# Kernel tuning notes

Hardware: AMD Instinct MI355X
Metric: run time of the kernel (lower is better)

Reference implementation:

```python
import jax, jax.numpy as jnp
import numpy as np

B, U, F = 32768, 256, 256  # batch, units, input features
LR = 0.01                  # inner_lr
EPS = 1e-3                 # TF LayerNormalization default epsilon


def _layer_norm(x, gamma, beta):
    m = jnp.mean(x, axis=-1, keepdims=True)
    v = jnp.var(x, axis=-1, keepdims=True)
    return (x - m) * jax.lax.rsqrt(v + EPS) * gamma + beta


def _enc(W1, b1, W2, b2, u):
    # mlp_2 inner encoder: Dense(4U, gelu-exact) -> Dense(U)
    return jax.nn.gelu(u @ W1 + b1, approximate=False) @ W2 + b2


def setup_inputs() -> dict:
    key = jax.random.key(0)
    ks = jax.random.split(key, 12)
    def w(k, shape):
        fan_in = shape[0]
        return jax.random.normal(k, shape, jnp.float32) / np.sqrt(fan_in)
    return {
        "x": jax.random.normal(ks[0], (B, F), jnp.float32),
        "h_prev": jax.random.normal(ks[1], (B, U), jnp.float32),
        "W_phi": w(ks[2], (F + U, U)), "b_phi": jnp.zeros((U,), jnp.float32),
        "W_psi": w(ks[3], (F + U, U)), "b_psi": jnp.zeros((U,), jnp.float32),
        "W1": w(ks[4], (U, 4 * U)), "b1": jnp.zeros((4 * U,), jnp.float32),
        "W2": w(ks[5], (4 * U, U)), "b2": jnp.zeros((U,), jnp.float32),
        "W_g": w(ks[6], (U, U)), "g_bias": jnp.zeros((U,), jnp.float32),
        "ln_gamma": jnp.ones((U,), jnp.float32), "ln_beta": jnp.zeros((U,), jnp.float32),
        "W_h": w(ks[7], (U, U)), "h_bias": jnp.zeros((U,), jnp.float32),
    }


def reference(x, h_prev, W_phi, b_phi, W_psi, b_psi, W1, b1, W2, b2,
              W_g, g_bias, ln_gamma, ln_beta, W_h, h_bias):
    z = jnp.concatenate([x, h_prev], axis=-1)          # [B, F+U]
    phi = z @ W_phi + b_phi                            # [B, U], also the inner target

    def inner_loss(params):
        W1_, b1_, W2_, b2_ = params
        r = _enc(W1_, b1_, W2_, b2_, phi) @ W_g + g_bias
        r = _layer_norm(r, ln_gamma, ln_beta)
        return jnp.mean(jnp.square(r - phi)), r

    params = (W1, b1, W2, b2)
    # inner_iterations = 1: one SGD step on the inner-encoder weights only
    (_, recon), grads = jax.value_and_grad(inner_loss, has_aux=True)(params)
    params = tuple(p - LR * g for p, g in zip(params, grads))

    psi = z @ W_psi + b_psi                            # [B, U]
    feat = _enc(*params, psi) + 0.1 * recon            # updated encoder on psi
    out = feat @ W_h + h_bias                          # new hidden / cell output
    return out
```

## Files before the change

### kernel.cpp

```cpp
#include <hip/hip_runtime.h>
#include <math.h>

#define B_N 32768
#define U_N 256
#define H_N 1024
#define LR_C 0.01f
#define EPS_C 1e-3f

typedef unsigned short ushort_t;
typedef unsigned int uint_t;
using frag8 = __attribute__((ext_vector_type(8))) short;
using f32x4 = __attribute__((ext_vector_type(4))) float;

__device__ __forceinline__ float erf_fast(float y) {
    float ay = fabsf(y);
    float t = __builtin_amdgcn_rcpf(fmaf(0.3275911f, ay, 1.0f));
    float p = fmaf(1.061405429f, t, -1.453152027f);
    p = fmaf(p, t, 1.421413741f);
    p = fmaf(p, t, -0.284496736f);
    p = fmaf(p, t, 0.254829592f);
    p = p * t;
    float e = __expf(-ay * ay);
    float r = fmaf(-p, e, 1.0f);
    return copysignf(r, y);
}
__device__ __forceinline__ float gelu_f(float x) {
    return 0.5f * x * (1.0f + erf_fast(x * 0.7071067811865475f));
}
__device__ __forceinline__ void gelu_pair(float x, float& g, float& d) {
    float ay = fabsf(x) * 0.7071067811865475f;
    float t = __builtin_amdgcn_rcpf(fmaf(0.3275911f, ay, 1.0f));
    float p = fmaf(1.061405429f, t, -1.453152027f);
    p = fmaf(p, t, 1.421413741f);
    p = fmaf(p, t, -0.284496736f);
    p = fmaf(p, t, 0.254829592f);
    p = p * t;
    float e = __expf(-ay * ay);
    float er = copysignf(fmaf(-p, e, 1.0f), x);
    float c = 0.5f * (1.0f + er);
    g = x * c;
    d = fmaf(x * 0.3989422804014327f, e, c);
}
__device__ __forceinline__ void splitf(float v, ushort_t& h, ushort_t& l) {
    uint_t u = __float_as_uint(v);
    h = (ushort_t)(u >> 16);
    float r = v - __uint_as_float(u & 0xFFFF0000u);
    uint_t ru = __float_as_uint(r);
    l = (ushort_t)((ru + 0x7FFFu + ((ru >> 16) & 1u)) >> 16);
}
__device__ __forceinline__ ushort_t cvt_rne(float v) {
    uint_t u = __float_as_uint(v);
    return (ushort_t)((u + 0x7FFFu + ((u >> 16) & 1u)) >> 16);
}
__device__ __forceinline__ float bf2f(ushort_t u) {
    return __uint_as_float((uint_t)u << 16);
}
__device__ __forceinline__ void unpack2(uint_t pa, uint_t pb, uint_t& hw, uint_t& lw) {
    hw = __builtin_amdgcn_perm(pb, pa, 0x07060302u);
    lw = __builtin_amdgcn_perm(pb, pa, 0x05040100u);
}
__device__ __forceinline__ size_t swz(int n, int k, int K) {
    return (size_t)n * K +
           (size_t)((k & ~31) | ((((k >> 3) & 3) ^ ((n >> 1) & 3)) << 3) | (k & 7));
}
__device__ __forceinline__ void gload16(const ushort_t* g, ushort_t* l) {
    __builtin_amdgcn_global_load_lds(
        (const __attribute__((address_space(1))) void*)g,
        (__attribute__((address_space(3))) void*)l, 16, 0, 0);
}

#define EPI_NONE 0
#define EPI_GELU 1
#define EPI_ADDS 3

#define BEP_P   0
#define BEP_PT  1
#define BEP_A1  2
#define BEP_DAT 3

template<int ACONCAT, int APACK, int EPI, int OPACK>
__global__ __launch_bounds__(256)
void mgemm_k(const float* A, const float* A2, const uint_t* __restrict__ AP,
             const ushort_t* __restrict__ BTh, const ushort_t* __restrict__ BTl,
             const float* __restrict__ bias, const ushort_t* __restrict__ Xr,
             float* C, uint_t* Cp,
             int M, int N, int K)
{
    __shared__ ushort_t Ah[128 * 40], Al[128 * 40];
    __shared__ ushort_t Bh[128 * 32], Bl[128 * 32];
    const int tid = threadIdx.x;
    const int m0 = blockIdx.x * 128, n0 = blockIdx.y * 128;
    const int lane = tid & 63, w = tid >> 6;
    const int wm = (w & 1) * 64, wn = (w >> 1) * 64;
    const int fr = lane & 15, fq = lane >> 4;
    const int sr = tid >> 1;
    const int sk = (tid & 1) * 16;

    f32x4 acc[4][4];
    #pragma unroll
    for (int i = 0; i < 4; i++)
        #pragma unroll
        for (int j = 0; j < 4; j++) acc[i][j] = (f32x4){0.f, 0.f, 0.f, 0.f};

    for (int k0 = 0; k0 < K; k0 += 32) {
        {
            const int r0w = w * 32;
            const size_t so = (size_t)(n0 + r0w + (lane >> 2)) * K + k0 + ((lane & 3) << 3);
            gload16(&BTh[so],                  &Bh[r0w * 32]);
            gload16(&BTh[so + (size_t)16 * K], &Bh[(r0w + 16) * 32]);
            gload16(&BTl[so],                  &Bl[r0w * 32]);
            gload16(&BTl[so + (size_t)16 * K], &Bl[(r0w + 16) * 32]);
        }
        if (APACK) {
            const uint_t* ap = AP + (size_t)(m0 + sr) * K + k0 + sk;
            uint4 p0 = *(const uint4*)(ap);
            uint4 p1 = *(const uint4*)(ap + 4);
            uint4 p2 = *(const uint4*)(ap + 8);
            uint4 p3 = *(const uint4*)(ap + 12);
            uint4 h0, h1, l0, l1;
            unpack2(p0.x, p0.y, h0.x, l0.x); unpack2(p0.z, p0.w, h0.y, l0.y);
            unpack2(p1.x, p1.y, h0.z, l0.z); unpack2(p1.z, p1.w, h0.w, l0.w);
            unpack2(p2.x, p2.y, h1.x, l1.x); unpack2(p2.z, p2.w, h1.y, l1.y);
            unpack2(p3.x, p3.y, h1.z, l1.z); unpack2(p3.z, p3.w, h1.w, l1.w);
            *(uint4*)&Ah[sr * 40 + sk]     = h0;
            *(uint4*)&Ah[sr * 40 + sk + 8] = h1;
            *(uint4*)&Al[sr * 40 + sk]     = l0;
            *(uint4*)&Al[sr * 40 + sk + 8] = l1;
        } else {
            #pragma unroll
            for (int g = 0; g < 2; g++) {
                uint4 qh, qa;
                uint_t ph[4], pl[4];
                #pragma unroll
                for (int c = 0; c < 2; c++) {
                    const int ak = k0 + sk + g * 8 + c * 4;
                    const float* ap;
                    if (ACONCAT) ap = (ak < 256) ? (A + (size_t)(m0 + sr) * 256 + ak)
                                                 : (A2 + (size_t)(m0 + sr) * 256 + (ak - 256));
                    else         ap = A + (size_t)(m0 + sr) * K + ak;
                    float4 v = *(const float4*)ap;
                    ushort_t h0,h1,h2,h3,l0,l1,l2,l3;
                    splitf(v.x,h0,l0); splitf(v.y,h1,l1); splitf(v.z,h2,l2); splitf(v.w,h3,l3);
                    ph[c*2]   = (uint_t)h0 | ((uint_t)h1 << 16);
                    ph[c*2+1] = (uint_t)h2 | ((uint_t)h3 << 16);
                    pl[c*2]   = (uint_t)l0 | ((uint_t)l1 << 16);
                    pl[c*2+1] = (uint_t)l2 | ((uint_t)l3 << 16);
                }
                qh.x = ph[0]; qh.y = ph[1]; qh.z = ph[2]; qh.w = ph[3];
                qa.x = pl[0]; qa.y = pl[1]; qa.z = pl[2]; qa.w = pl[3];
                *(uint4*)&Ah[sr * 40 + sk + g * 8] = qh;
                *(uint4*)&Al[sr * 40 + sk + g * 8] = qa;
            }
        }
        __syncthreads();

        frag8 afh[4], afl[4], bfh[4], bfl[4];
        #pragma unroll
        for (int i = 0; i < 4; i++) {
            const int ar = wm + i * 16 + fr;
            afh[i] = *(frag8*)&Ah[ar * 40 + fq * 8];
            afl[i] = *(frag8*)&Al[ar * 40 + fq * 8];
        }
        #pragma unroll
        for (int j = 0; j < 4; j++) {
            const int br = wn + j * 16 + fr;
            const int bs = br * 32 + ((fq ^ ((br >> 1) & 3)) << 3);
            bfh[j] = *(frag8*)&Bh[bs];
            bfl[j] = *(frag8*)&Bl[bs];
        }
        #pragma unroll
        for (int i = 0; i < 4; i++)
            #pragma unroll
            for (int j = 0; j < 4; j++) {
                acc[i][j] = __builtin_amdgcn_mfma_f32_16x16x32_bf16(afh[i], bfh[j], acc[i][j], 0, 0, 0);
                acc[i][j] = __builtin_amdgcn_mfma_f32_16x16x32_bf16(afh[i], bfl[j], acc[i][j], 0, 0, 0);
                acc[i][j] = __builtin_amdgcn_mfma_f32_16x16x32_bf16(afl[i], bfh[j], acc[i][j], 0, 0, 0);
            }
        __syncthreads();
    }

    float bv[4] = {0.f, 0.f, 0.f, 0.f};
    if (bias != nullptr)
        #pragma unroll
        for (int j = 0; j < 4; j++) bv[j] = bias[n0 + wn + j * 16 + fr];
    #pragma unroll
    for (int i = 0; i < 4; i++)
        #pragma unroll
        for (int j = 0; j < 4; j++) {
            const int col = n0 + wn + j * 16 + fr;
            #pragma unroll
            for (int r = 0; r < 4; r++) {
                const int row = m0 + wm + i * 16 + fq * 4 + r;
                const size_t off = (size_t)row * N + col;
                float c = acc[i][j][r] + bv[j];
                if (EPI == EPI_GELU)      c = gelu_f(c);
                else if (EPI == EPI_ADDS) c = c + 0.1f * bf2f(Xr[off]);
                if (OPACK) {
                    ushort_t h, l;
                    splitf(c, h, l);
                    Cp[off] = ((uint_t)h << 16) | (uint_t)l;
                } else {
                    C[off] = c;
                }
            }
        }
}

template<int ACONCAT, int BEP>
__global__ __launch_bounds__(256)
void bgemm_k(const void* Av, const float* A2f, const ushort_t* __restrict__ BTh,
             const float* __restrict__ bias, const ushort_t* __restrict__ GpIn,
             ushort_t* Crm, ushort_t* Cct, ushort_t* GpOut, float* dbsum,
             int M, int N, int K)
{
    __shared__ ushort_t Ah[128 * 40];
    __shared__ ushort_t Bh[128 * 32];
    const int tid = threadIdx.x;
    const int m0 = blockIdx.x * 128, n0 = blockIdx.y * 128;
    const int lane = tid & 63, w = tid >> 6;
    const int wm = (w & 1) * 64, wn = (w >> 1) * 64;
    const int fr = lane & 15, fq = lane >> 4;
    const int sr = tid >> 1;
    const int sk = (tid & 1) * 16;

    f32x4 acc[4][4];
    #pragma unroll
    for (int i = 0; i < 4; i++)
        #pragma unroll
        for (int j = 0; j < 4; j++) acc[i][j] = (f32x4){0.f, 0.f, 0.f, 0.f};

    for (int k0 = 0; k0 < K; k0 += 32) {
        {
            const int r0w = w * 32;
            const size_t so = (size_t)(n0 + r0w + (lane >> 2)) * K + k0 + ((lane & 3) << 3);
            gload16(&BTh[so],                  &Bh[r0w * 32]);
            gload16(&BTh[so + (size_t)16 * K], &Bh[(r0w + 16) * 32]);
        }
        if (ACONCAT) {
            const float* A = (const float*)Av;
            #pragma unroll
            for (int g = 0; g < 2; g++) {
                uint_t ph[4];
                #pragma unroll
                for (int c = 0; c < 2; c++) {
                    const int ak = k0 + sk + g * 8 + c * 4;
                    const float* ap = (ak < 256) ? (A + (size_t)(m0 + sr) * 256 + ak)
                                                 : (A2f + (size_t)(m0 + sr) * 256 + (ak - 256));
                    float4 v = *(const float4*)ap;
                    ph[c*2]   = (uint_t)cvt_rne(v.x) | ((uint_t)cvt_rne(v.y) << 16);
                    ph[c*2+1] = (uint_t)cvt_rne(v.z) | ((uint_t)cvt_rne(v.w) << 16);
                }
                uint4 q; q.x = ph[0]; q.y = ph[1]; q.z = ph[2]; q.w = ph[3];
                *(uint4*)&Ah[sr * 40 + sk + g * 8] = q;
            }
        } else {
            const ushort_t* A = (const ushort_t*)Av;
            const size_t ao = (size_t)(m0 + sr) * K + k0 + sk;
            *(uint4*)&Ah[sr * 40 + sk]     = *(const uint4*)&A[ao];
            *(uint4*)&Ah[sr * 40 + sk + 8] = *(const uint4*)&A[ao + 8];
        }
        __syncthreads();

        frag8 af[4], bf[4];
        #pragma unroll
        for (int i = 0; i < 4; i++) af[i] = *(frag8*)&Ah[(wm + i * 16 + fr) * 40 + fq * 8];
        #pragma unroll
        for (int j = 0; j < 4; j++) {
            const int br = wn + j * 16 + fr;
            bf[j] = *(frag8*)&Bh[br * 32 + ((fq ^ ((br >> 1) & 3)) << 3)];
        }
        #pragma unroll
        for (int i = 0; i < 4; i++)
            #pragma unroll
            for (int j = 0; j < 4; j++)
                acc[i][j] = __builtin_amdgcn_mfma_f32_16x16x32_bf16(af[i], bf[j], acc[i][j], 0, 0, 0);
        __syncthreads();
    }

    float bv[4] = {0.f, 0.f, 0.f, 0.f};
    if (bias != nullptr)
        #pragma unroll
        for (int j = 0; j < 4; j++) bv[j] = bias[n0 + wn + j * 16 + fr];
    float cs[4] = {0.f, 0.f, 0.f, 0.f};
    #pragma unroll
    for (int i = 0; i < 4; i++)
        #pragma unroll
        for (int j = 0; j < 4; j++) {
            const int col = n0 + wn + j * 16 + fr;
            const int rowb = m0 + wm + i * 16 + fq * 4;
            float v[4];
            #pragma unroll
            for (int r = 0; r < 4; r++) v[r] = acc[i][j][r] + bv[j];
            if (BEP == BEP_A1) {
                ushort_t gc[4];
                #pragma unroll
                for (int r = 0; r < 4; r++) {
                    float g, d;
                    gelu_pair(v[r], g, d);
                    gc[r] = cvt_rne(g);
                    Crm[(size_t)(rowb + r) * N + col] = gc[r];
                    GpOut[(size_t)(rowb + r) * N + col] = cvt_rne(d);
                }
                uint_t p0 = (uint_t)gc[0] | ((uint_t)gc[1] << 16);
                uint_t p1 = (uint_t)gc[2] | ((uint_t)gc[3] << 16);
                *(uint2*)&Cct[(size_t)col * M + rowb] = (uint2){p0, p1};
            } else if (BEP == BEP_DAT) {
                ushort_t dc[4];
                #pragma unroll
                for (int r = 0; r < 4; r++) {
                    float pr = v[r] * bf2f(GpIn[(size_t)(rowb + r) * N + col]);
                    dc[r] = cvt_rne(pr);
                    cs[j] += pr;
                }
                uint_t p0 = (uint_t)dc[0] | ((uint_t)dc[1] << 16);
                uint_t p1 = (uint_t)dc[2] | ((uint_t)dc[3] << 16);
                *(uint2*)&Cct[(size_t)col * M + rowb] = (uint2){p0, p1};
            } else {
                ushort_t cc[4];
                #pragma unroll
                for (int r = 0; r < 4; r++) {
                    cc[r] = cvt_rne(v[r]);
                    Crm[(size_t)(rowb + r) * N + col] = cc[r];
                }
                cs[j] += v[0] + v[1] + v[2] + v[3];
                if (BEP == BEP_PT) {
                    uint_t p0 = (uint_t)cc[0] | ((uint_t)cc[1] << 16);
                    uint_t p1 = (uint_t)cc[2] | ((uint_t)cc[3] << 16);
                    *(uint2*)&Cct[(size_t)col * M + rowb] = (uint2){p0, p1};
                }
            }
        }
    if (dbsum != nullptr) {
        #pragma unroll
        for (int j = 0; j < 4; j++) {
            float s = cs[j];
            s += __shfl_xor(s, 16);
            s += __shfl_xor(s, 32);
            if (fq == 0) atomicAdd(&dbsum[n0 + wn + j * 16 + fr], s);
        }
    }
}

__global__ __launch_bounds__(256)
void wgrad_k(const ushort_t* __restrict__ AT, const ushort_t* __restrict__ BTt,
             float* C, int M, int N, int KA, int kofsA, int KB, int kofsB, int KC)
{
    __shared__ ushort_t Ah[128 * 40];
    __shared__ ushort_t Bh[128 * 40];
    const int tid = threadIdx.x;
    const int m0 = blockIdx.x * 128, n0 = blockIdx.y * 128;
    const int kbA = kofsA + blockIdx.z * KC;
    const int kbB = kofsB + blockIdx.z * KC;
    const int lane = tid & 63, w = tid >> 6;
    const int wm = (w & 1) * 64, wn = (w >> 1) * 64;
    const int fr = lane & 15, fq = lane >> 4;
    const int sr = tid >> 1;
    const int sk = (tid & 1) * 16;

    f32x4 acc[4][4];
    #pragma unroll
    for (int i = 0; i < 4; i++)
        #pragma unroll
        for (int j = 0; j < 4; j++) acc[i][j] = (f32x4){0.f, 0.f, 0.f, 0.f};

    for (int k0 = 0; k0 < KC; k0 += 32) {
        const size_t ao = (size_t)(m0 + sr) * KA + kbA + k0 + sk;
        *(uint4*)&Ah[sr * 40 + sk]     = *(const uint4*)&AT[ao];
        *(uint4*)&Ah[sr * 40 + sk + 8] = *(const uint4*)&AT[ao + 8];
        const size_t bo = (size_t)(n0 + sr) * KB + kbB + k0 + sk;
        *(uint4*)&Bh[sr * 40 + sk]     = *(const uint4*)&BTt[bo];
        *(uint4*)&Bh[sr * 40 + sk + 8] = *(const uint4*)&BTt[bo + 8];
        __syncthreads();

        frag8 af[4], bf[4];
        #pragma unroll
        for (int i = 0; i < 4; i++) af[i] = *(frag8*)&Ah[(wm + i * 16 + fr) * 40 + fq * 8];
        #pragma unroll
        for (int j = 0; j < 4; j++) bf[j] = *(frag8*)&Bh[(wn + j * 16 + fr) * 40 + fq * 8];
        #pragma unroll
        for (int i = 0; i < 4; i++)
            #pragma unroll
            for (int j = 0; j < 4; j++)
                acc[i][j] = __builtin_amdgcn_mfma_f32_16x16x32_bf16(af[i], bf[j], acc[i][j], 0, 0, 0);
        __syncthreads();
    }
    #pragma unroll
    for (int i = 0; i < 4; i++)
        #pragma unroll
        for (int j = 0; j < 4; j++) {
            const int col = n0 + wn + j * 16 + fr;
            #pragma unroll
            for (int r = 0; r < 4; r++) {
                const int row = m0 + wm + i * 16 + fq * 4 + r;
                atomicAdd(&C[(size_t)row * N + col], acc[i][j][r]);
            }
        }
}

__global__ __launch_bounds__(256)
void ln_bf_k(const ushort_t* r0, const ushort_t* __restrict__ phi,
             const float* __restrict__ gamma, const float* __restrict__ beta,
             ushort_t* recon, ushort_t* dr0)
{
    const int lane = threadIdx.x & 63;
    const int wv = threadIdx.x >> 6;
    const int row = blockIdx.x * 4 + wv;
    const size_t base = (size_t)row * U_N + (lane << 2);

    uint2 xu = *(const uint2*)(r0 + base);
    uint2 pu = *(const uint2*)(phi + base);
    float xs[4] = { bf2f((ushort_t)(xu.x & 0xFFFF)), bf2f((ushort_t)(xu.x >> 16)),
                    bf2f((ushort_t)(xu.y & 0xFFFF)), bf2f((ushort_t)(xu.y >> 16)) };
    float ps[4] = { bf2f((ushort_t)(pu.x & 0xFFFF)), bf2f((ushort_t)(pu.x >> 16)),
                    bf2f((ushort_t)(pu.y & 0xFFFF)), bf2f((ushort_t)(pu.y >> 16)) };
    float s = xs[0] + xs[1] + xs[2] + xs[3];
    float sq = xs[0]*xs[0] + xs[1]*xs[1] + xs[2]*xs[2] + xs[3]*xs[3];
    #pragma unroll
    for (int o = 32; o > 0; o >>= 1) { s += __shfl_xor(s, o); sq += __shfl_xor(sq, o); }
    const float m   = s * (1.0f / U_N);
    const float var = sq * (1.0f / U_N) - m * m;
    const float inv = rsqrtf(var + EPS_C);

    float4 gv = *(const float4*)(gamma + (lane << 2));
    float4 bvv = *(const float4*)(beta + (lane << 2));
    float gs[4] = {gv.x, gv.y, gv.z, gv.w};
    float bs[4] = {bvv.x, bvv.y, bvv.z, bvv.w};
    float rh[4], dh[4], rc[4];
    float s1 = 0.f, s2 = 0.f;
    const float gscale = 2.0f / ((float)B_N * (float)U_N);
    #pragma unroll
    for (int j = 0; j < 4; j++) {
        rh[j] = (xs[j] - m) * inv;
        rc[j] = rh[j] * gs[j] + bs[j];
        float g2 = gscale * (rc[j] - ps[j]);
        dh[j] = g2 * gs[j];
        s1 += dh[j];
        s2 += dh[j] * rh[j];
    }
    #pragma unroll
    for (int o = 32; o > 0; o >>= 1) { s1 += __shfl_xor(s1, o); s2 += __shfl_xor(s2, o); }
    const float mu1 = s1 * (1.0f / U_N);
    const float mu2 = s2 * (1.0f / U_N);
    ushort_t oc[4], dc[4];
    #pragma unroll
    for (int j = 0; j < 4; j++) {
        oc[j] = cvt_rne(rc[j]);
        dc[j] = cvt_rne(inv * (dh[j] - mu1 - rh[j] * mu2));
    }
    *(uint2*)(recon + base) = (uint2){ (uint_t)oc[0] | ((uint_t)oc[1] << 16),
                                       (uint_t)oc[2] | ((uint_t)oc[3] << 16) };
    *(uint2*)(dr0 + base)   = (uint2){ (uint_t)dc[0] | ((uint_t)dc[1] << 16),
                                       (uint_t)dc[2] | ((uint_t)dc[3] << 16) };
}

template<int HASL>
__global__ __launch_bounds__(256)
void tsplit_k(const float* __restrict__ W, ushort_t* __restrict__ Th,
              ushort_t* __restrict__ Tl, int R, int C)
{
    __shared__ float t[64][65];
    const int tid = threadIdx.x;
    const int R0 = blockIdx.x * 64, C0 = blockIdx.y * 64;
    const int c = tid & 63, rb = (tid >> 6) * 16;
    for (int i = 0; i < 16; i++)
        t[rb + i][c] = W[(size_t)(R0 + rb + i) * C + C0 + c];
    __syncthreads();
    const int orr = tid & 63, ob = (tid >> 6) * 16;
    for (int i = 0; i < 16; i++) {
        const int oc = ob + i;
        ushort_t h, l;
        splitf(t[orr][oc], h, l);
        const size_t d = swz(C0 + oc, R0 + orr, R);
        Th[d] = h;
        if (HASL) Tl[d] = l;
    }
}

__global__ __launch_bounds__(256)
void tupd_k(const float* __restrict__ W, const float* __restrict__ dW,
            ushort_t* __restrict__ Th, ushort_t* __restrict__ Tl, int R, int C)
{
    __shared__ float t[64][65];
    const int tid = threadIdx.x;
    const int R0 = blockIdx.x * 64, C0 = blockIdx.y * 64;
    const int c = tid & 63, rb = (tid >> 6) * 16;
    for (int i = 0; i < 16; i++) {
        const size_t o = (size_t)(R0 + rb + i) * C + C0 + c;
        t[rb + i][c] = W[o] - LR_C * dW[o];
    }
    __syncthreads();
    const int orr = tid & 63, ob = (tid >> 6) * 16;
    for (int i = 0; i < 16; i++) {
        const int oc = ob + i;
        ushort_t h, l;
        splitf(t[orr][oc], h, l);
        const size_t d = swz(C0 + oc, R0 + orr, R);
        Th[d] = h;
        Tl[d] = l;
    }
}

__global__ __launch_bounds__(256)
void scvt_k(const float* __restrict__ W, ushort_t* __restrict__ Th, int n4)
{
    const int i = blockIdx.x * 256 + threadIdx.x;
    if (i >= n4) return;
    float4 v = *(const float4*)(W + (size_t)i * 4);
    const int f = i * 4;
    const int row = f >> 8, col = f & 255;
    uint2 ph;
    ph.x = (uint_t)cvt_rne(v.x) | ((uint_t)cvt_rne(v.y) << 16);
    ph.y = (uint_t)cvt_rne(v.z) | ((uint_t)cvt_rne(v.w) << 16);
    *(uint2*)&Th[swz(row, col, 256)] = ph;
}

__global__ __launch_bounds__(256)
void wcmul_k(const float* __restrict__ W2, const float* __restrict__ Wg,
             float* __restrict__ Wc)
{
    const int i = blockIdx.x;
    const int j = threadIdx.x;
    float s = 0.f;
    for (int k = 0; k < 256; k++)
        s = fmaf(W2[i * 256 + k], Wg[k * 256 + j], s);
    Wc[i * 256 + j] = s;
}
__global__ __launch_bounds__(256)
void bcmul_k(const float* __restrict__ b2, const float* __restrict__ Wg,
             const float* __restrict__ gb, float* __restrict__ bc)
{
    const int j = threadIdx.x;
    float s = gb[j];
    for (int k = 0; k < 256; k++)
        s = fmaf(b2[k], Wg[k * 256 + j], s);
    bc[j] = s;
}

__global__ __launch_bounds__(256)
void bupd_k(const float* __restrict__ b1, const float* __restrict__ db1,
            const float* __restrict__ b2, const float* __restrict__ db2,
            float* __restrict__ b1u, float* __restrict__ b2u)
{
    const int i = blockIdx.x * 256 + threadIdx.x;
    if (i < H_N) b1u[i] = b1[i] - LR_C * db1[i];
    else if (i < H_N + U_N) b2u[i - H_N] = b2[i - H_N] - LR_C * db2[i - H_N];
}

extern "C" void kernel_launch(void* const* d_in, const int* in_sizes, int n_in,
                              void* d_out, int out_size, void* d_ws, size_t ws_size,
                              hipStream_t stream)
{
    const float* x      = (const float*)d_in[0];
    const float* h_prev = (const float*)d_in[1];
    const float* W_phi  = (const float*)d_in[2];
    const float* b_phi  = (const float*)d_in[3];
    const float* W_psi  = (const float*)d_in[4];
    const float* b_psi  = (const float*)d_in[5];
    const float* W1     = (const float*)d_in[6];
    const float* b1     = (const float*)d_in[7];
    const float* W2     = (const float*)d_in[8];
    const float* b2     = (const float*)d_in[9];
    const float* W_g    = (const float*)d_in[10];
    const float* g_bias = (const float*)d_in[11];
    const float* gamma  = (const float*)d_in[12];
    const float* beta   = (const float*)d_in[13];
    const float* W_h    = (const float*)d_in[14];
    const float* h_bias = (const float*)d_in[15];
    float* out = (float*)d_out;

    const size_t BU = (size_t)B_N * U_N;
    const size_t UH = (size_t)U_N * H_N;

    float* ws  = (float*)d_ws;
    float* dW1 = ws;
    float* db1 = dW1 + UH;
    float* dW2 = db1 + H_N;
    float* db2 = dW2 + UH;
    float* b1u = db2 + U_N;
    float* b2u = b1u + H_N;
    float* bc  = b2u + U_N;
    float* Wc  = bc + U_N;
    ushort_t* us = (ushort_t*)(((uintptr_t)(Wc + UH) + 15) & ~(uintptr_t)15);
    ushort_t* WphiT_h = us;
    ushort_t* WpsiT_h = WphiT_h + 131072;     ushort_t* WpsiT_l = WpsiT_h + 131072;
    ushort_t* WcT_h   = WpsiT_l + 131072;
    ushort_t* W1T_h   = WcT_h + 262144;
    ushort_t* W2s_h   = W1T_h + 262144;
    ushort_t* Wgs_h   = W2s_h + 262144;
    ushort_t* W1uT_h  = Wgs_h + 65536;        ushort_t* W1uT_l = W1uT_h + 262144;
    ushort_t* W2uT_h  = W1uT_l + 262144;      ushort_t* W2uT_l = W2uT_h + 262144;
    ushort_t* WhT_h   = W2uT_l + 262144;      ushort_t* WhT_l  = WhT_h + 65536;
    ushort_t* phi_bf  = WhT_l + 65536;
    ushort_t* phiT_bf = phi_bf + BU;
    ushort_t* recon_bf= phiT_bf + BU;
    ushort_t* chunk0  = recon_bf + BU;
    const size_t P_bytes = (size_t)((char*)chunk0 - (char*)d_ws);

    int GA = 2;
    while (GA < 256 && P_bytes + (size_t)(B_N / GA) * 10240 + (1 << 20) > ws_size) GA *= 2;
    size_t region = (size_t)(B_N / GA) * 10240;
    int GC = 1;
    while (GC < 256) {
        size_t cC = (size_t)(B_N / GC) * 6144;
        size_t r = cC > region ? cC : region;
        if (P_bytes + r + (1 << 20) <= ws_size) { region = r; break; }
        GC *= 2;
    }
    const int BcA = B_N / GA;
    const int BcC = B_N / GC;
    const int KC = (BcA >= 8192) ? 512 : ((BcA >= 1024) ? BcA / 16 : BcA);
    const int Z  = BcA / KC;

    ushort_t* g1  = chunk0;
    ushort_t* gp  = g1  + (size_t)BcA * H_N;
    ushort_t* g1T = gp  + (size_t)BcA * H_N;
    ushort_t* daT = g1T + (size_t)BcA * H_N;
    ushort_t* e_b = daT + (size_t)BcA * H_N;
    ushort_t* r0b = e_b + (size_t)BcA * U_N;
    ushort_t* deb = r0b + (size_t)BcA * U_N;
    ushort_t* deT = deb + (size_t)BcA * U_N;
    uint_t* psi_p  = (uint_t*)chunk0;
    uint_t* h2_p   = psi_p + (size_t)BcC * U_N;
    uint_t* feat_p = h2_p  + (size_t)BcC * H_N;

    hipMemsetAsync(dW1, 0, (2 * UH + H_N + U_N) * sizeof(float), stream);

    dim3 blk(256);
    tsplit_k<0><<<dim3(8, 4),  blk, 0, stream>>>(W_phi, WphiT_h, nullptr, 512, 256);
    tsplit_k<1><<<dim3(8, 4),  blk, 0, stream>>>(W_psi, WpsiT_h, WpsiT_l, 512, 256);
    tsplit_k<0><<<dim3(4, 16), blk, 0, stream>>>(W1, W1T_h, nullptr, 256, 1024);
    tsplit_k<1><<<dim3(4, 4),  blk, 0, stream>>>(W_h, WhT_h, WhT_l, 256, 256);
    scvt_k<<<dim3(256), blk, 0, stream>>>(W2, W2s_h, 65536);
    scvt_k<<<dim3(64),  blk, 0, stream>>>(W_g, Wgs_h, 16384);
    wcmul_k<<<dim3(1024), blk, 0, stream>>>(W2, W_g, Wc);
    bcmul_k<<<dim3(1), blk, 0, stream>>>(b2, W_g, g_bias, bc);
    tsplit_k<0><<<dim3(16, 4), blk, 0, stream>>>(Wc, WcT_h, nullptr, 1024, 256);

    bgemm_k<1, BEP_PT><<<dim3(B_N / 128, 2), blk, 0, stream>>>(
        x, h_prev, WphiT_h, b_phi, nullptr, phi_bf, phiT_bf, nullptr, nullptr,
        B_N, U_N, 512);

    for (int c = 0; c < GA; c++) {
        const size_t off = (size_t)c * BcA;
        const ushort_t* phic = phi_bf + off * U_N;
        bgemm_k<0, BEP_A1><<<dim3(BcA / 128, 8), blk, 0, stream>>>(
            phic, nullptr, W1T_h, b1, nullptr, g1, g1T, gp, nullptr, BcA, H_N, U_N);
        bgemm_k<0, BEP_P><<<dim3(BcA / 128, 2), blk, 0, stream>>>(
            g1, nullptr, WcT_h, bc, nullptr, r0b, nullptr, nullptr, nullptr,
            BcA, U_N, H_N);
        ln_bf_k<<<dim3(BcA / 4), blk, 0, stream>>>(r0b, phic, gamma, beta,
                                                   recon_bf + off * U_N, r0b);
        bgemm_k<0, BEP_PT><<<dim3(BcA / 128, 2), blk, 0, stream>>>(
            r0b, nullptr, Wgs_h, nullptr, nullptr, deb, deT, nullptr, db2,
            BcA, U_N, U_N);
        bgemm_k<0, BEP_DAT><<<dim3(BcA / 128, 8), blk, 0, stream>>>(
            deb, nullptr, W2s_h, nullptr, gp, nullptr, daT, nullptr, db1,
            BcA, H_N, U_N);
        wgrad_k<<<dim3(8, 2, Z), blk, 0, stream>>>(g1T, deT, dW2, H_N, U_N,
                                                   BcA, 0, BcA, 0, KC);
        wgrad_k<<<dim3(2, 8, Z), blk, 0, stream>>>(phiT_bf, daT, dW1, U_N, H_N,
                                                   B_N, (int)off, BcA, 0, KC);
    }

    bupd_k<<<dim3(5), blk, 0, stream>>>(b1, db1, b2, db2, b1u, b2u);
    tupd_k<<<dim3(4, 16), blk, 0, stream>>>(W1, dW1, W1uT_h, W1uT_l, 256, 1024);
    tupd_k<<<dim3(16, 4), blk, 0, stream>>>(W2, dW2, W2uT_h, W2uT_l, 1024, 256);

    for (int c = 0; c < GC; c++) {
        const size_t off = (size_t)c * BcC;
        mgemm_k<1, 0, EPI_NONE, 1><<<dim3(BcC / 128, 2), blk, 0, stream>>>(
            x + off * 256, h_prev + off * U_N, nullptr,
            WpsiT_h, WpsiT_l, b_psi, nullptr,
            nullptr, psi_p, BcC, U_N, 512);
        mgemm_k<0, 1, EPI_GELU, 1><<<dim3(BcC / 128, 8), blk, 0, stream>>>(
            nullptr, nullptr, psi_p,
            W1uT_h, W1uT_l, b1u, nullptr,
            nullptr, h2_p, BcC, H_N, U_N);
        mgemm_k<0, 1, EPI_ADDS, 1><<<dim3(BcC / 128, 2), blk, 0, stream>>>(
            nullptr, nullptr, h2_p,
            W2uT_h, W2uT_l, b2u, recon_bf + off * U_N,
            nullptr, feat_p, BcC, U_N, H_N);
        mgemm_k<0, 1, EPI_NONE, 0><<<dim3(BcC / 128, 2), blk, 0, stream>>>(
            nullptr, nullptr, feat_p,
            WhT_h, WhT_l, h_bias, nullptr,
            out + off * U_N, nullptr, BcC, U_N, U_N);
    }
}
```

Before: 845.5 us.

## Fold W_g into backward pass using precomputed Wc and reassociated weight gradient

Drops the per-chunk GEMM that multiplied the layernorm gradient by W_g^T. The activation gradient is now computed directly with the precomputed Wc = W2·W_g. dW2 is obtained by accumulating G2 = g1^T·dr over the batch and multiplying by W_g^T once at the end, with db2 taken from column sums of dr. The layernorm kernel also writes a transposed copy of dr through shared memory. This removes one B×256×256 GEMM per chunk at the cost of a small colsum kernel, the transposed write, and two tiny post-loop kernels. Numerics change slightly because bf16 rounding happens at different points.

```diff
diff --git a/kernel.cpp b/kernel.cpp
--- a/kernel.cpp
+++ b/kernel.cpp
@@ -400,8 +400,9 @@
 __global__ __launch_bounds__(256)
 void ln_bf_k(const ushort_t* r0, const ushort_t* __restrict__ phi,
              const float* __restrict__ gamma, const float* __restrict__ beta,
-             ushort_t* recon, ushort_t* dr0)
-{
+             ushort_t* recon, ushort_t* dr0, ushort_t* dr0T, int LD)
+{
+    __shared__ ushort_t tds[4][256];
     const int lane = threadIdx.x & 63;
     const int wv = threadIdx.x >> 6;
     const int row = blockIdx.x * 4 + wv;
@@ -449,8 +450,40 @@
     }
     *(uint2*)(recon + base) = (uint2){ (uint_t)oc[0] | ((uint_t)oc[1] << 16),
                                        (uint_t)oc[2] | ((uint_t)oc[3] << 16) };
-    *(uint2*)(dr0 + base)   = (uint2){ (uint_t)dc[0] | ((uint_t)dc[1] << 16),
-                                       (uint_t)dc[2] | ((uint_t)dc[3] << 16) };
+    uint2 dpk = (uint2){ (uint_t)dc[0] | ((uint_t)dc[1] << 16),
+                         (uint_t)dc[2] | ((uint_t)dc[3] << 16) };
+    *(uint2*)(dr0 + base) = dpk;
+    *(uint2*)&tds[wv][lane << 2] = dpk;
+    __syncthreads();
+    const int col = threadIdx.x;
+    uint_t p0 = (uint_t)tds[0][col] | ((uint_t)tds[1][col] << 16);
+    uint_t p1 = (uint_t)tds[2][col] | ((uint_t)tds[3][col] << 16);
+    *(uint2*)&dr0T[(size_t)col * LD + blockIdx.x * 4] = (uint2){p0, p1};
+}
+
+__global__ __launch_bounds__(256)
+void colsum_rm_k(const ushort_t* __restrict__ D, float* cs, int rows)
+{
+    __shared__ float red[4][256];
+    const int tid = threadIdx.x;
+    const int cg = (tid & 63) << 2;
+    const int rg = tid >> 6;
+    float a0 = 0.f, a1 = 0.f, a2 = 0.f, a3 = 0.f;
+    const int rpb = rows / gridDim.x;
+    const int r0 = blockIdx.x * rpb;
+    for (int r = r0 + rg; r < r0 + rpb; r += 4) {
+        uint2 q = *(const uint2*)&D[(size_t)r * 256 + cg];
+        a0 += bf2f((ushort_t)(q.x & 0xFFFF)); a1 += bf2f((ushort_t)(q.x >> 16));
+        a2 += bf2f((ushort_t)(q.y & 0xFFFF)); a3 += bf2f((ushort_t)(q.y >> 16));
+    }
+    red[rg][cg]     = a0;
+    red[rg][cg + 1] = a1;
+    red[rg][cg + 2] = a2;
+    red[rg][cg + 3] = a3;
+    __syncthreads();
+    const int c = tid;
+    float ssum = red[0][c] + red[1][c] + red[2][c] + red[3][c];
+    atomicAdd(&cs[c], ssum);
 }
 
 template<int HASL>
@@ -534,6 +567,27 @@
     for (int k = 0; k < 256; k++)
         s = fmaf(b2[k], Wg[k * 256 + j], s);
     bc[j] = s;
+}
+__global__ __launch_bounds__(256)
+void dw2f_k(const float* __restrict__ G2, const float* __restrict__ Wg,
+            float* __restrict__ dW2)
+{
+    const int i = blockIdx.x;
+    const int u = threadIdx.x;
+    float s = 0.f;
+    for (int v = 0; v < 256; v++)
+        s = fmaf(G2[i * 256 + v], Wg[u * 256 + v], s);
+    dW2[i * 256 + u] = s;
+}
+__global__ __launch_bounds__(256)
+void db2f_k(const float* __restrict__ cs2, const float* __restrict__ Wg,
+            float* __restrict__ db2)
+{
+    const int u = threadIdx.x;
+    float s = 0.f;
+    for (int v = 0; v < 256; v++)
+        s = fmaf(cs2[v], Wg[u * 256 + v], s);
+    db2[u] = s;
 }
 
 __global__ __launch_bounds__(256)
@@ -574,20 +628,21 @@
     float* ws  = (float*)d_ws;
     float* dW1 = ws;
     float* db1 = dW1 + UH;
-    float* dW2 = db1 + H_N;
-    float* db2 = dW2 + UH;
-    float* b1u = db2 + U_N;
+    float* G2  = db1 + H_N;
+    float* cs2 = G2 + UH;
+    float* b1u = cs2 + U_N;
     float* b2u = b1u + H_N;
     float* bc  = b2u + U_N;
     float* Wc  = bc + U_N;
-    ushort_t* us = (ushort_t*)(((uintptr_t)(Wc + UH) + 15) & ~(uintptr_t)15);
+    float* dW2f= Wc + UH;
+    float* db2f= dW2f + UH;
+    ushort_t* us = (ushort_t*)(((uintptr_t)(db2f + U_N) + 15) & ~(uintptr_t)15);
     ushort_t* WphiT_h = us;
     ushort_t* WpsiT_h = WphiT_h + 131072;     ushort_t* WpsiT_l = WpsiT_h + 131072;
     ushort_t* WcT_h   = WpsiT_l + 131072;
     ushort_t* W1T_h   = WcT_h + 262144;
-    ushort_t* W2s_h   = W1T_h + 262144;
-    ushort_t* Wgs_h   = W2s_h + 262144;
-    ushort_t* W1uT_h  = Wgs_h + 65536;        ushort_t* W1uT_l = W1uT_h + 262144;
+    ushort_t* Wcs_h   = W1T_h + 262144;
+    ushort_t* W1uT_h  = Wcs_h + 262144;       ushort_t* W1uT_l = W1uT_h + 262144;
     ushort_t* W2uT_h  = W1uT_l + 262144;      ushort_t* W2uT_l = W2uT_h + 262144;
     ushort_t* WhT_h   = W2uT_l + 262144;      ushort_t* WhT_l  = WhT_h + 65536;
     ushort_t* phi_bf  = WhT_l + 65536;
@@ -618,7 +673,7 @@
     ushort_t* e_b = daT + (size_t)BcA * H_N;
     ushort_t* r0b = e_b + (size_t)BcA * U_N;
     ushort_t* deb = r0b + (size_t)BcA * U_N;
-    ushort_t* deT = deb + (size_t)BcA * U_N;
+    ushort_t* drT = deb + (size_t)BcA * U_N;
     uint_t* psi_p  = (uint_t*)chunk0;
     uint_t* h2_p   = psi_p + (size_t)BcC * U_N;
     uint_t* feat_p = h2_p  + (size_t)BcC * H_N;
@@ -630,11 +685,10 @@
     tsplit_k<1><<<dim3(8, 4),  blk, 0, stream>>>(W_psi, WpsiT_h, WpsiT_l, 512, 256);
     tsplit_k<0><<<dim3(4, 16), blk, 0, stream>>>(W1, W1T_h, nullptr, 256, 1024);
     tsplit_k<1><<<dim3(4, 4),  blk, 0, stream>>>(W_h, WhT_h, WhT_l, 256, 256);
-    scvt_k<<<dim3(256), blk, 0, stream>>>(W2, W2s_h, 65536);
-    scvt_k<<<dim3(64),  blk, 0, stream>>>(W_g, Wgs_h, 16384);
     wcmul_k<<<dim3(1024), blk, 0, stream>>>(W2, W_g, Wc);
     bcmul_k<<<dim3(1), blk, 0, stream>>>(b2, W_g, g_bias, bc);
     tsplit_k<0><<<dim3(16, 4), blk, 0, stream>>>(Wc, WcT_h, nullptr, 1024, 256);
+    scvt_k<<<dim3(256), blk, 0, stream>>>(Wc, Wcs_h, 65536);
 
     bgemm_k<1, BEP_PT><<<dim3(B_N / 128, 2), blk, 0, stream>>>(
         x, h_prev, WphiT_h, b_phi, nullptr, phi_bf, phiT_bf, nullptr, nullptr,
@@ -649,22 +703,23 @@
             g1, nullptr, WcT_h, bc, nullptr, r0b, nullptr, nullptr, nullptr,
             BcA, U_N, H_N);
         ln_bf_k<<<dim3(BcA / 4), blk, 0, stream>>>(r0b, phic, gamma, beta,
-                                                   recon_bf + off * U_N, r0b);
-        bgemm_k<0, BEP_PT><<<dim3(BcA / 128, 2), blk, 0, stream>>>(
-            r0b, nullptr, Wgs_h, nullptr, nullptr, deb, deT, nullptr, db2,
-            BcA, U_N, U_N);
+                                                   recon_bf + off * U_N, r0b,
+                                                   drT, BcA);
         bgemm_k<0, BEP_DAT><<<dim3(BcA / 128, 8), blk, 0, stream>>>(
-            deb, nullptr, W2s_h, nullptr, gp, nullptr, daT, nullptr, db1,
+            r0b, nullptr, Wcs_h, nullptr, gp, nullptr, daT, nullptr, db1,
             BcA, H_N, U_N);
-        wgrad_k<<<dim3(8, 2, Z), blk, 0, stream>>>(g1T, deT, dW2, H_N, U_N,
+        colsum_rm_k<<<dim3(32), blk, 0, stream>>>(r0b, cs2, BcA);
+        wgrad_k<<<dim3(8, 2, Z), blk, 0, stream>>>(g1T, drT, G2, H_N, U_N,
                                                    BcA, 0, BcA, 0, KC);
         wgrad_k<<<dim3(2, 8, Z), blk, 0, stream>>>(phiT_bf, daT, dW1, U_N, H_N,
                                                    B_N, (int)off, BcA, 0, KC);
     }
 
-    bupd_k<<<dim3(5), blk, 0, stream>>>(b1, db1, b2, db2, b1u, b2u);
+    dw2f_k<<<dim3(1024), blk, 0, stream>>>(G2, W_g, dW2f);
+    db2f_k<<<dim3(1), blk, 0, stream>>>(cs2, W_g, db2f);
+    bupd_k<<<dim3(5), blk, 0, stream>>>(b1, db1, b2, db2f, b1u, b2u);
     tupd_k<<<dim3(4, 16), blk, 0, stream>>>(W1, dW1, W1uT_h, W1uT_l, 256, 1024);
-    tupd_k<<<dim3(16, 4), blk, 0, stream>>>(W2, dW2, W2uT_h, W2uT_l, 1024, 256);
+    tupd_k<<<dim3(16, 4), blk, 0, stream>>>(W2, dW2f, W2uT_h, W2uT_l, 1024, 256);
 
     for (int c = 0; c < GC; c++) {
         const size_t off = (size_t)c * BcC;
```

Result: slower. 1.045 ms (+23.6%).
